# Optimization experiments

Measured on AMD Instinct MI355X. Metric: run time of the kernel, lower is better.

## Reference

```python
import jax, jax.numpy as jnp
import numpy as np

B, T, H, C = 64, 512, 1024, 21  # batch, seq_len, hidden_size, num_labels


def setup_inputs() -> dict:
    key = jax.random.key(0)
    ks = jax.random.split(key, 7)
    hidden_states = jax.random.normal(ks[0], (B, T, H), dtype=jnp.float32)
    lengths = jax.random.randint(ks[1], (B,), 1, T + 1)  # at least 1 valid token
    attention_mask = jnp.arange(T)[None, :] < lengths[:, None]  # [B,T] bool, contiguous prefix
    labels = jax.random.randint(ks[2], (B, T), 0, C)
    # classifier params (nn.Linear(H, C))
    W = jax.random.normal(ks[3], (H, C), dtype=jnp.float32) * 0.02
    b = jnp.zeros((C,), dtype=jnp.float32)
    # CRF params (torchcrf init: uniform(-0.1, 0.1))
    transitions = jax.random.uniform(ks[4], (C, C), minval=-0.1, maxval=0.1, dtype=jnp.float32)
    start_transitions = jax.random.uniform(ks[5], (C,), minval=-0.1, maxval=0.1, dtype=jnp.float32)
    end_transitions = jax.random.uniform(ks[6], (C,), minval=-0.1, maxval=0.1, dtype=jnp.float32)
    return {
        "hidden_states": hidden_states,
        "W": W,
        "b": b,
        "transitions": transitions,
        "start_transitions": start_transitions,
        "end_transitions": end_transitions,
        "attention_mask": attention_mask,
        "labels": labels,
    }


def _crf_nll(emissions, tags, mask, transitions, start_transitions, end_transitions):
    """Mean negative log-likelihood of torchcrf CRF(batch_first=True, reduction='mean')."""
    maskf = mask.astype(emissions.dtype)
    # ---- numerator: score of the gold tag path ----
    em_tag = jnp.take_along_axis(emissions, tags[..., None], axis=2)[..., 0]  # [B,T]
    trans_score = transitions[tags[:, :-1], tags[:, 1:]]                      # [B,T-1]
    num = (start_transitions[tags[:, 0]] + em_tag[:, 0]
           + jnp.sum((trans_score + em_tag[:, 1:]) * maskf[:, 1:], axis=1))
    last_idx = jnp.sum(mask.astype(jnp.int32), axis=1) - 1                    # [B]
    last_tag = jnp.take_along_axis(tags, last_idx[:, None], axis=1)[:, 0]
    num = num + end_transitions[last_tag]
    # ---- denominator: forward algorithm (log partition) ----
    alpha0 = start_transitions[None, :] + emissions[:, 0]                     # [B,C]

    def step(alpha, xs):
        em_t, m_t = xs  # [B,C], [B]
        nxt = jax.nn.logsumexp(alpha[:, :, None] + transitions[None, :, :] + em_t[:, None, :], axis=1)
        return jnp.where(m_t[:, None], nxt, alpha), None

    xs = (jnp.swapaxes(emissions[:, 1:], 0, 1), jnp.swapaxes(mask[:, 1:], 0, 1))
    alphaT, _ = jax.lax.scan(step, alpha0, xs)
    logZ = jax.nn.logsumexp(alphaT + end_transitions[None, :], axis=1)        # [B]
    llh = num - logZ
    return -jnp.mean(llh)


def reference(hidden_states, W, b, transitions, start_transitions, end_transitions,
              attention_mask, labels):
    # dropout is identity at inference; emissions = Linear(hidden)
    emissions = jnp.einsum('bth,hc->btc', hidden_states, W) + b              # [B,T,C]
    # mask logic from the module: attention_mask & (labels != -100); mask[:,0] = True
    mask = attention_mask & (labels != -100)
    mask = mask.at[:, 0].set(True)
    loss = _crf_nll(emissions, labels, mask, transitions, start_transitions, end_transitions)
    return emissions, loss
```

## Files before the change

kernel.cpp:

```cpp
#include <hip/hip_runtime.h>

#define BB 64
#define TT 512
#define HH 1024
#define CC 21
#define NROWS (BB*TT)
#define WPAD 24
#define TSTR 65
#define TSZ  (64*TSTR)

__global__ __launch_bounds__(512) void emis_gemm(const float* __restrict__ hs,
                                                 const float* __restrict__ W,
                                                 const float* __restrict__ bias,
                                                 float* __restrict__ out) {
  __shared__ float lds[32896];
  float* Wl   = lds;
  float* tile = lds + 24576;
  const int tid  = threadIdx.x;
  const int lane = tid & 63;
  const int w    = __builtin_amdgcn_readfirstlane(tid >> 6);
  const int row0 = blockIdx.x * 64;

  if (blockIdx.x == 0 && tid == 0) out[(size_t)NROWS * CC] = 0.f;

  for (int i = 0; i < 42; ++i) {
    int idx = tid + i * 512;
    int k = idx / 21;
    int c = idx - k * 21;
    Wl[k * WPAD + c] = W[idx];
  }

  float acc[CC];
#pragma unroll
  for (int c = 0; c < CC; ++c) acc[c] = 0.f;

  const int r_  = tid >> 4, c4_ = tid & 15;
  const int r2_ = (tid + 512) >> 4;

  float4 buf0 = *reinterpret_cast<const float4*>(hs + (size_t)(row0 + r_ ) * HH + c4_ * 4);
  float4 buf1 = *reinterpret_cast<const float4*>(hs + (size_t)(row0 + r2_) * HH + c4_ * 4);
  {
    float* t0 = &tile[r_  * TSTR + c4_ * 4];
    float* t1 = &tile[r2_ * TSTR + c4_ * 4];
    t0[0] = buf0.x; t0[1] = buf0.y; t0[2] = buf0.z; t0[3] = buf0.w;
    t1[0] = buf1.x; t1[1] = buf1.y; t1[2] = buf1.z; t1[3] = buf1.w;
  }
  __syncthreads();

  for (int chunk = 0; chunk < 16; ++chunk) {
    float* cur = tile + (chunk & 1) * TSZ;
    float* nxt = tile + ((chunk + 1) & 1) * TSZ;
    if (chunk < 15) {
      const int k0n = (chunk + 1) * 64;
      buf0 = *reinterpret_cast<const float4*>(hs + (size_t)(row0 + r_ ) * HH + k0n + c4_ * 4);
      buf1 = *reinterpret_cast<const float4*>(hs + (size_t)(row0 + r2_) * HH + k0n + c4_ * 4);
    }
    const float* wl = Wl + (chunk * 64 + w * 8) * WPAD;
#pragma unroll
    for (int kk = 0; kk < 8; ++kk) {
      float x = cur[lane * TSTR + w * 8 + kk];
      const float4* wr = reinterpret_cast<const float4*>(wl + kk * WPAD);
      float4 w0 = wr[0], w1 = wr[1], w2 = wr[2], w3 = wr[3], w4 = wr[4], w5 = wr[5];
      acc[ 0] = fmaf(x, w0.x, acc[ 0]);
      acc[ 1] = fmaf(x, w0.y, acc[ 1]);
      acc[ 2] = fmaf(x, w0.z, acc[ 2]);
      acc[ 3] = fmaf(x, w0.w, acc[ 3]);
      acc[ 4] = fmaf(x, w1.x, acc[ 4]);
      acc[ 5] = fmaf(x, w1.y, acc[ 5]);
      acc[ 6] = fmaf(x, w1.z, acc[ 6]);
      acc[ 7] = fmaf(x, w1.w, acc[ 7]);
      acc[ 8] = fmaf(x, w2.x, acc[ 8]);
      acc[ 9] = fmaf(x, w2.y, acc[ 9]);
      acc[10] = fmaf(x, w2.z, acc[10]);
      acc[11] = fmaf(x, w2.w, acc[11]);
      acc[12] = fmaf(x, w3.x, acc[12]);
      acc[13] = fmaf(x, w3.y, acc[13]);
      acc[14] = fmaf(x, w3.z, acc[14]);
      acc[15] = fmaf(x, w3.w, acc[15]);
      acc[16] = fmaf(x, w4.x, acc[16]);
      acc[17] = fmaf(x, w4.y, acc[17]);
      acc[18] = fmaf(x, w4.z, acc[18]);
      acc[19] = fmaf(x, w4.w, acc[19]);
      acc[20] = fmaf(x, w5.x, acc[20]);
    }
    if (chunk < 15) {
      float* t0 = &nxt[r_  * TSTR + c4_ * 4];
      float* t1 = &nxt[r2_ * TSTR + c4_ * 4];
      t0[0] = buf0.x; t0[1] = buf0.y; t0[2] = buf0.z; t0[3] = buf0.w;
      t1[0] = buf1.x; t1[1] = buf1.y; t1[2] = buf1.z; t1[3] = buf1.w;
    }
    __syncthreads();
  }

  if (w > 0) {
#pragma unroll
    for (int c = 0; c < CC; ++c)
      Wl[(w - 1) * 1344 + lane * CC + c] = acc[c];
  }
  __syncthreads();
  if (w == 0) {
#pragma unroll
    for (int c = 0; c < CC; ++c) {
      float v = acc[c] + bias[c];
#pragma unroll
      for (int q = 0; q < 7; ++q) v += Wl[q * 1344 + lane * CC + c];
      Wl[9408 + lane * CC + c] = v;
    }
  }
  __syncthreads();
  for (int idx = tid; idx < 1344; idx += 512)
    out[(size_t)row0 * CC + idx] = Wl[9408 + idx];
}

__global__ __launch_bounds__(128) void crf_kernel(const float* __restrict__ em,
                                                  const float* __restrict__ trans,
                                                  const float* __restrict__ startT,
                                                  const float* __restrict__ endT,
                                                  const int* __restrict__ att,
                                                  const int* __restrict__ labels,
                                                  float* __restrict__ loss) {
  const int b    = blockIdx.x;
  const int tid  = threadIdx.x;
  const int wave = tid >> 6;
  const int lane = tid & 63;
  __shared__ float sh_num;
  __shared__ int   sh_len;

  const float L2E = 1.4426950408889634f;
  const float LN2 = 0.6931471805599453f;

  if (wave == 1) {
    int cnt = 0;
    for (int t = lane; t < TT; t += 64) {
      bool m = (t == 0) || ((att[b * TT + t] != 0) && (labels[b * TT + t] != -100));
      cnt += m ? 1 : 0;
    }
#pragma unroll
    for (int off = 32; off >= 1; off >>= 1) cnt += __shfl_down(cnt, off);
    cnt = __shfl(cnt, 0);

    float s = 0.f;
    for (int t = lane + 1; t < TT; t += 64) {
      bool m = (att[b * TT + t] != 0) && (labels[b * TT + t] != -100);
      if (m) {
        int tp = labels[b * TT + t - 1], tc = labels[b * TT + t];
        s += trans[tp * CC + tc] + em[((size_t)b * TT + t) * CC + tc];
      }
    }
#pragma unroll
    for (int off = 32; off >= 1; off >>= 1) s += __shfl_down(s, off);
    if (lane == 0) {
      int tag0 = labels[b * TT];
      int lastTag = labels[b * TT + cnt - 1];
      s += startT[tag0] + em[((size_t)b * TT) * CC + tag0] + endT[lastTag];
      sh_num = s;
      sh_len = cnt;
    }
  }

  const int j = lane < CC ? lane : CC - 1;
  float E[CC];
  float beta = 0.f, endE = 0.f;
  if (wave == 0) {
#pragma unroll
    for (int i = 0; i < CC; ++i)
      E[i] = __builtin_amdgcn_exp2f(trans[i * CC + j] * L2E);
    beta = __builtin_amdgcn_exp2f((startT[j] + em[((size_t)b * TT) * CC + j]) * L2E);
    endE = __builtin_amdgcn_exp2f(endT[j] * L2E);
  }
  __syncthreads();

  if (wave == 0) {
    const int len = sh_len;
    int ksum = 0;

    float sb[CC];
#pragma unroll
    for (int i = 0; i < CC; ++i)
      sb[i] = __int_as_float(__builtin_amdgcn_readlane(__float_as_int(beta), i));

    const float* emB = em + (size_t)b * TT * CC;

    auto step = [&](float em_v) {
      float pm = __builtin_amdgcn_exp2f(em_v * L2E);
      int ef = (__float_as_int(sb[0]) >> 23) & 255;
      ksum += ef - 127;
      float pms = pm * __int_as_float((254 - ef) << 23);
      float c0 = 0.f, c1 = 0.f, c2 = 0.f;
#pragma unroll
      for (int i = 0; i < CC; i += 3) c0 = fmaf(sb[i], E[i], c0);
#pragma unroll
      for (int i = 1; i < CC; i += 3) c1 = fmaf(sb[i], E[i], c1);
#pragma unroll
      for (int i = 2; i < CC; i += 3) c2 = fmaf(sb[i], E[i], c2);
      beta = ((c0 + c1) + c2) * pms;
#pragma unroll
      for (int i = 0; i < CC; ++i)
        sb[i] = __int_as_float(__builtin_amdgcn_readlane(__float_as_int(beta), i));
    };

    float r[8];
#pragma unroll
    for (int u = 0; u < 8; ++u) {
      int tt = 1 + u; if (tt > len - 1) tt = len - 1;
      r[u] = emB[(size_t)tt * CC + j];
    }

    int t = 1;
    for (; t + 8 <= len; t += 8) {
#pragma unroll
      for (int u = 0; u < 8; ++u) {
        int tp = t + u + 8; if (tp > len - 1) tp = len - 1;
        float rn = emB[(size_t)tp * CC + j];
        step(r[u]);
        r[u] = rn;
      }
    }
    for (; t < len; ++t) {
      step(r[0]);
#pragma unroll
      for (int u = 0; u < 7; ++u) r[u] = r[u + 1];
    }

    float v = (lane < CC) ? beta * endE : 0.f;
#pragma unroll
    for (int off = 32; off >= 1; off >>= 1) v += __shfl_xor(v, off);
    if (lane == 0) {
      float logZ = (float)ksum * LN2 + LN2 * __builtin_amdgcn_logf(v);
      atomicAdd(loss, -(sh_num - logZ) * (1.0f / 64.0f));
    }
  }
}

extern "C" void kernel_launch(void* const* d_in, const int* in_sizes, int n_in,
                              void* d_out, int out_size, void* d_ws, size_t ws_size,
                              hipStream_t stream) {
  const float* hs     = (const float*)d_in[0];
  const float* W      = (const float*)d_in[1];
  const float* bias   = (const float*)d_in[2];
  const float* trans  = (const float*)d_in[3];
  const float* startT = (const float*)d_in[4];
  const float* endT   = (const float*)d_in[5];
  const int*   att    = (const int*)d_in[6];
  const int*   labels = (const int*)d_in[7];
  float* out = (float*)d_out;

  emis_gemm<<<dim3(512), dim3(512), 0, stream>>>(hs, W, bias, out);
  crf_kernel<<<dim3(64), dim3(128), 0, stream>>>(out, trans, startT, endT, att,
                                                 labels, out + (size_t)NROWS * CC);
}
```

Before: 283.3 us.

## Stream hidden rows directly into registers and read W via uniform global loads

The emission GEMM no longer stages W and hidden-state tiles in LDS. Each lane now owns one row and each wave owns a 128-wide K slice, which it reads with per-lane float4 loads and software double-buffering. W is read from global memory at wave-uniform addresses, which should compile to scalar loads. This removes the LDS traffic and barriers from the main loop and cuts shared memory to the cross-wave reduction buffer, with launch bounds raised to allow 4 blocks per CU. The trade-off is strided, per-lane global access patterns, which may coalesce less well than the previous tiled loads.

```diff
diff --git a/kernel.cpp b/kernel.cpp
--- a/kernel.cpp
+++ b/kernel.cpp
@@ -5,97 +5,56 @@
 #define HH 1024
 #define CC 21
 #define NROWS (BB*TT)
-#define WPAD 24
-#define TSTR 65
-#define TSZ  (64*TSTR)
-
-__global__ __launch_bounds__(512) void emis_gemm(const float* __restrict__ hs,
-                                                 const float* __restrict__ W,
-                                                 const float* __restrict__ bias,
-                                                 float* __restrict__ out) {
-  __shared__ float lds[32896];
-  float* Wl   = lds;
-  float* tile = lds + 24576;
+
+__global__ __launch_bounds__(512, 4) void emis_gemm(const float* __restrict__ hs,
+                                                    const float* __restrict__ W,
+                                                    const float* __restrict__ bias,
+                                                    float* __restrict__ out) {
+  __shared__ float red[7 * 1344];
   const int tid  = threadIdx.x;
   const int lane = tid & 63;
   const int w    = __builtin_amdgcn_readfirstlane(tid >> 6);
-  const int row0 = blockIdx.x * 64;
+  const int row  = blockIdx.x * 64 + lane;
+  const int k0   = w * 128;
 
   if (blockIdx.x == 0 && tid == 0) out[(size_t)NROWS * CC] = 0.f;
 
-  for (int i = 0; i < 42; ++i) {
-    int idx = tid + i * 512;
-    int k = idx / 21;
-    int c = idx - k * 21;
-    Wl[k * WPAD + c] = W[idx];
-  }
-
   float acc[CC];
 #pragma unroll
   for (int c = 0; c < CC; ++c) acc[c] = 0.f;
 
-  const int r_  = tid >> 4, c4_ = tid & 15;
-  const int r2_ = (tid + 512) >> 4;
-
-  float4 buf0 = *reinterpret_cast<const float4*>(hs + (size_t)(row0 + r_ ) * HH + c4_ * 4);
-  float4 buf1 = *reinterpret_cast<const float4*>(hs + (size_t)(row0 + r2_) * HH + c4_ * 4);
-  {
-    float* t0 = &tile[r_  * TSTR + c4_ * 4];
-    float* t1 = &tile[r2_ * TSTR + c4_ * 4];
-    t0[0] = buf0.x; t0[1] = buf0.y; t0[2] = buf0.z; t0[3] = buf0.w;
-    t1[0] = buf1.x; t1[1] = buf1.y; t1[2] = buf1.z; t1[3] = buf1.w;
-  }
-  __syncthreads();
-
-  for (int chunk = 0; chunk < 16; ++chunk) {
-    float* cur = tile + (chunk & 1) * TSZ;
-    float* nxt = tile + ((chunk + 1) & 1) * TSZ;
-    if (chunk < 15) {
-      const int k0n = (chunk + 1) * 64;
-      buf0 = *reinterpret_cast<const float4*>(hs + (size_t)(row0 + r_ ) * HH + k0n + c4_ * 4);
-      buf1 = *reinterpret_cast<const float4*>(hs + (size_t)(row0 + r2_) * HH + k0n + c4_ * 4);
-    }
-    const float* wl = Wl + (chunk * 64 + w * 8) * WPAD;
-#pragma unroll
-    for (int kk = 0; kk < 8; ++kk) {
-      float x = cur[lane * TSTR + w * 8 + kk];
-      const float4* wr = reinterpret_cast<const float4*>(wl + kk * WPAD);
-      float4 w0 = wr[0], w1 = wr[1], w2 = wr[2], w3 = wr[3], w4 = wr[4], w5 = wr[5];
-      acc[ 0] = fmaf(x, w0.x, acc[ 0]);
-      acc[ 1] = fmaf(x, w0.y, acc[ 1]);
-      acc[ 2] = fmaf(x, w0.z, acc[ 2]);
-      acc[ 3] = fmaf(x, w0.w, acc[ 3]);
-      acc[ 4] = fmaf(x, w1.x, acc[ 4]);
-      acc[ 5] = fmaf(x, w1.y, acc[ 5]);
-      acc[ 6] = fmaf(x, w1.z, acc[ 6]);
-      acc[ 7] = fmaf(x, w1.w, acc[ 7]);
-      acc[ 8] = fmaf(x, w2.x, acc[ 8]);
-      acc[ 9] = fmaf(x, w2.y, acc[ 9]);
-      acc[10] = fmaf(x, w2.z, acc[10]);
-      acc[11] = fmaf(x, w2.w, acc[11]);
-      acc[12] = fmaf(x, w3.x, acc[12]);
-      acc[13] = fmaf(x, w3.y, acc[13]);
-      acc[14] = fmaf(x, w3.z, acc[14]);
-      acc[15] = fmaf(x, w3.w, acc[15]);
-      acc[16] = fmaf(x, w4.x, acc[16]);
-      acc[17] = fmaf(x, w4.y, acc[17]);
-      acc[18] = fmaf(x, w4.z, acc[18]);
-      acc[19] = fmaf(x, w4.w, acc[19]);
-      acc[20] = fmaf(x, w5.x, acc[20]);
-    }
-    if (chunk < 15) {
-      float* t0 = &nxt[r_  * TSTR + c4_ * 4];
-      float* t1 = &nxt[r2_ * TSTR + c4_ * 4];
-      t0[0] = buf0.x; t0[1] = buf0.y; t0[2] = buf0.z; t0[3] = buf0.w;
-      t1[0] = buf1.x; t1[1] = buf1.y; t1[2] = buf1.z; t1[3] = buf1.w;
-    }
-    __syncthreads();
+  const float* p  = hs + (size_t)row * HH + k0;
+  const float* Wp = W  + (size_t)k0 * CC;
+
+  float4 X[4], X2[4];
+#pragma unroll
+  for (int j = 0; j < 4; ++j)
+    X[j] = *reinterpret_cast<const float4*>(p + 4 * j);
+
+  for (int g = 0; g < 8; ++g) {
+    if (g < 7) {
+#pragma unroll
+      for (int j = 0; j < 4; ++j)
+        X2[j] = *reinterpret_cast<const float4*>(p + (g + 1) * 16 + 4 * j);
+    }
+    const float* wg = Wp + g * 16 * CC;
+#pragma unroll
+    for (int kk = 0; kk < 16; ++kk) {
+      const float x = ((kk & 3) == 0) ? X[kk >> 2].x :
+                      ((kk & 3) == 1) ? X[kk >> 2].y :
+                      ((kk & 3) == 2) ? X[kk >> 2].z : X[kk >> 2].w;
+      const float* wr = wg + kk * CC;
+#pragma unroll
+      for (int c = 0; c < CC; ++c) acc[c] = fmaf(x, wr[c], acc[c]);
+    }
+#pragma unroll
+    for (int j = 0; j < 4; ++j) X[j] = X2[j];
   }
 
   if (w > 0) {
 #pragma unroll
     for (int c = 0; c < CC; ++c)
-      Wl[(w - 1) * 1344 + lane * CC + c] = acc[c];
+      red[(w - 1) * 1344 + lane * CC + c] = acc[c];
   }
   __syncthreads();
   if (w == 0) {
@@ -103,13 +62,13 @@
     for (int c = 0; c < CC; ++c) {
       float v = acc[c] + bias[c];
 #pragma unroll
-      for (int q = 0; q < 7; ++q) v += Wl[q * 1344 + lane * CC + c];
-      Wl[9408 + lane * CC + c] = v;
+      for (int q = 0; q < 7; ++q) v += red[q * 1344 + lane * CC + c];
+      red[lane * CC + c] = v;
     }
   }
   __syncthreads();
   for (int idx = tid; idx < 1344; idx += 512)
-    out[(size_t)row0 * CC + idx] = Wl[9408 + idx];
+    out[(size_t)blockIdx.x * 1344 + idx] = red[idx];
 }
 
 __global__ __launch_bounds__(128) void crf_kernel(const float* __restrict__ em,
```

After: 295.0 us. 4.1% more time.
